# Optimization experiments

Hardware: AMD Instinct MI355X
Metric: run time of the kernel (lower is better)

Reference implementation:

```python
import jax, jax.numpy as jnp
import numpy as np

B, T, D, H = 4, 2048, 1024, 16
HD = D // H  # head_dim = 64


def setup_inputs() -> dict:
    key = jax.random.key(0)
    ks = jax.random.split(key, 7)
    x = jax.random.normal(ks[0], (B, T, D), dtype=jnp.float32)
    engagement = jax.random.uniform(ks[1], (B, T), dtype=jnp.float32)
    mask = jax.random.uniform(ks[2], (B, T)) < 0.1  # True = masked-out key
    s = 1.0 / np.sqrt(D)
    qkv_w = jax.random.normal(ks[3], (3 * D, D), dtype=jnp.float32) * s
    qkv_b = jax.random.normal(ks[4], (3 * D,), dtype=jnp.float32) * 0.02
    out_w = jax.random.normal(ks[5], (D, D), dtype=jnp.float32) * s
    out_b = jax.random.normal(ks[6], (D,), dtype=jnp.float32) * 0.02
    return {"x": x, "engagement": engagement, "mask": mask,
            "qkv_w": qkv_w, "qkv_b": qkv_b, "out_w": out_w, "out_b": out_b}


def reference(x, engagement, mask, qkv_w, qkv_b, out_w, out_b):
    b, t, d = x.shape
    qkv = x @ qkv_w.T + qkv_b                       # [B,T,3D]
    q, k, v = jnp.split(qkv, 3, axis=-1)
    # [B,T,D] -> [B,H,T,HD]
    to_heads = lambda a: a.reshape(b, t, H, HD).transpose(0, 2, 1, 3)
    q, k, v = to_heads(q), to_heads(k), to_heads(v)
    attn = jnp.einsum('bhqd,bhkd->bhqk', q, k) / jnp.sqrt(jnp.float32(HD))
    log_g = jnp.log(jnp.clip(engagement, 1e-6))     # [B,T] per-key bias
    attn = attn + log_g[:, None, None, :]
    attn = jnp.where(mask[:, None, None, :], jnp.float32(-1e9), attn)
    p = jax.nn.softmax(attn, axis=-1)
    o = jnp.einsum('bhqk,bhkd->bhqd', p, v)         # [B,H,T,HD]
    o = o.transpose(0, 2, 1, 3).reshape(b, t, d)    # [B,T,D]
    return o @ out_w.T + out_b
```

## Files before the change

kernel.cpp:

```cpp
#include <hip/hip_runtime.h>
#include <math.h>

#define B_  4
#define T_  2048
#define D_  1024
#define H_  16
#define HD_ 64

typedef unsigned short ushort_t;
typedef unsigned int uint_t;
typedef __attribute__((ext_vector_type(8))) short bf16x8;
typedef __attribute__((ext_vector_type(4))) float f32x4;

#define SC_LOG2 0.1803368801111243f

__device__ inline ushort_t f2bf(float f) {
  uint_t u = __float_as_uint(f);
  u += 0x7fffu + ((u >> 16) & 1u);
  return (ushort_t)(u >> 16);
}
__device__ inline ushort_t f2bf_fast(float f) {
  return (ushort_t)((__float_as_uint(f) + 0x8000u) >> 16);
}

__device__ inline void gload_lds16(const ushort_t* g, ushort_t* l) {
  __builtin_amdgcn_global_load_lds(
      (const __attribute__((address_space(1))) unsigned int*)g,
      (__attribute__((address_space(3))) unsigned int*)l, 16, 0, 0);
}

__global__ __launch_bounds__(256) void cvt_bf16(const float* __restrict__ in,
                                                ushort_t* __restrict__ out, int n) {
  int i = (blockIdx.x * 256 + threadIdx.x) * 4;
  if (i + 3 < n) {
    float4 v = *(const float4*)(in + i);
    uint_t lo = (uint_t)f2bf(v.x) | ((uint_t)f2bf(v.y) << 16);
    uint_t hi = (uint_t)f2bf(v.z) | ((uint_t)f2bf(v.w) << 16);
    *(uint2*)(out + i) = make_uint2(lo, hi);
  }
}

__global__ __launch_bounds__(256) void bias_prep(const float* __restrict__ eng,
                                                 const int* __restrict__ mask,
                                                 float* __restrict__ biasA, int n) {
  int i = blockIdx.x * 256 + threadIdx.x;
  if (i < n) biasA[i] = mask[i] ? -1e30f : __log2f(fmaxf(eng[i], 1e-6f));
}

template <int WRITE_BF16>
__global__ __launch_bounds__(256) void gemm_bf16(
    const ushort_t* __restrict__ A, const ushort_t* __restrict__ Bm,
    const float* __restrict__ bias, void* __restrict__ Cout,
    int M, int N, int K) {
  __shared__ __align__(16) ushort_t Ls[8192];
  ushort_t* As = Ls;
  ushort_t* Bs = Ls + 4096;
  const int tid = threadIdx.x;
  const int w = tid >> 6, lane = tid & 63;
  const int l15 = lane & 15, quad = lane >> 4;
  const int wm = w >> 1, wn = w & 1;
  const int m0 = blockIdx.y * 128, n0 = blockIdx.x * 128;

  f32x4 acc[4][4];
#pragma unroll
  for (int a = 0; a < 4; ++a)
#pragma unroll
    for (int b = 0; b < 4; ++b) acc[a][b] = (f32x4){0.f, 0.f, 0.f, 0.f};

  const int sr = lane >> 2;
  const int gc = (lane & 3) ^ ((sr >> 1) & 3);

  for (int k0 = 0; k0 < K; k0 += 32) {
    __syncthreads();
#pragma unroll
    for (int u = 0; u < 2; ++u) {
      int row = w * 32 + u * 16 + sr;
      gload_lds16(A + (size_t)(m0 + row) * K + k0 + gc * 8,
                  &As[(w * 32 + u * 16) * 32]);
      gload_lds16(Bm + (size_t)(n0 + row) * K + k0 + gc * 8,
                  &Bs[(w * 32 + u * 16) * 32]);
    }
    __syncthreads();
    bf16x8 af[4], bf[4];
#pragma unroll
    for (int mb = 0; mb < 4; ++mb) {
      int row = wm * 64 + mb * 16 + l15;
      int p = quad ^ ((l15 >> 1) & 3);
      af[mb] = *(const bf16x8*)(&As[row * 32 + p * 8]);
    }
#pragma unroll
    for (int nb = 0; nb < 4; ++nb) {
      int row = wn * 64 + nb * 16 + l15;
      int p = quad ^ ((l15 >> 1) & 3);
      bf[nb] = *(const bf16x8*)(&Bs[row * 32 + p * 8]);
    }
#pragma unroll
    for (int mb = 0; mb < 4; ++mb)
#pragma unroll
      for (int nb = 0; nb < 4; ++nb)
        acc[mb][nb] = __builtin_amdgcn_mfma_f32_16x16x32_bf16(
            af[mb], bf[nb], acc[mb][nb], 0, 0, 0);
  }

  float bb[4];
#pragma unroll
  for (int nb = 0; nb < 4; ++nb) bb[nb] = bias[n0 + wn * 64 + nb * 16 + l15];

  if (WRITE_BF16) {
    ushort_t* Cb = (ushort_t*)Cout;
#pragma unroll
    for (int mb = 0; mb < 4; ++mb) {
      __syncthreads();
#pragma unroll
      for (int nb = 0; nb < 4; ++nb)
#pragma unroll
        for (int i = 0; i < 4; ++i) {
          float v = acc[mb][nb][i] + bb[nb];
          Ls[(wm * 16 + quad * 4 + i) * 136 + wn * 64 + nb * 16 + l15] =
              f2bf_fast(v);
        }
      __syncthreads();
      int lr = tid >> 3, c = tid & 7;
      size_t gr = (size_t)(m0 + (lr >> 4) * 64 + mb * 16 + (lr & 15));
      uint4 v0 = *(const uint4*)&Ls[lr * 136 + c * 16];
      uint4 v1 = *(const uint4*)&Ls[lr * 136 + c * 16 + 8];
      *(uint4*)&Cb[gr * N + n0 + c * 16] = v0;
      *(uint4*)&Cb[gr * N + n0 + c * 16 + 8] = v1;
    }
  } else {
    float* Cf = (float*)Cout;
#pragma unroll
    for (int mb = 0; mb < 4; ++mb)
#pragma unroll
      for (int i = 0; i < 4; ++i) {
        size_t row = (size_t)(m0 + wm * 64 + mb * 16 + quad * 4 + i);
#pragma unroll
        for (int nb = 0; nb < 4; ++nb)
          Cf[row * N + n0 + wn * 64 + nb * 16 + l15] = acc[mb][nb][i] + bb[nb];
      }
  }
}

__global__ __launch_bounds__(256) void attn_mfma(
    const ushort_t* __restrict__ qkv, const float* __restrict__ biasA,
    ushort_t* __restrict__ oat) {
  __shared__ __align__(16) ushort_t Kb[64 * 64];
  __shared__ __align__(16) ushort_t Vb[8 * 520];
  __shared__ __align__(16) ushort_t Pl[4][16 * 72];
  __shared__ float bsh[64];

  const int b = blockIdx.z, h = blockIdx.y;
  const int q0 = blockIdx.x * 64;
  const int tid = threadIdx.x;
  const int w = tid >> 6, lane = tid & 63;
  const int l15 = lane & 15, quad = lane >> 4;
  const size_t rs = 3 * D_;

  const ushort_t* qb =
      qkv + (size_t)(b * T_ + q0 + w * 16 + l15) * rs + h * HD_;
  bf16x8 qf0 = *(const bf16x8*)(qb + quad * 8);
  bf16x8 qf1 = *(const bf16x8*)(qb + 32 + quad * 8);

  f32x4 Oa[4];
#pragma unroll
  for (int nb = 0; nb < 4; ++nb) Oa[nb] = (f32x4){0.f, 0.f, 0.f, 0.f};
  float rsum[4] = {0.f, 0.f, 0.f, 0.f};

  const ushort_t* kbase = qkv + (size_t)(b * T_) * rs + D_ + h * HD_;
  const ushort_t* vbase = kbase + D_;
  const float* bptr = biasA + b * T_;
  ushort_t* pw = &Pl[w][0];

  const int kr = lane >> 3, kc = lane & 7;
  const int kgc = kc ^ kr;

  for (int k0 = 0; k0 < T_; k0 += 64) {
    __syncthreads();
#pragma unroll
    for (int u = 0; u < 2; ++u) {
      int key = w * 16 + u * 8 + kr;
      gload_lds16(kbase + (size_t)(k0 + key) * rs + kgc * 8,
                  &Kb[(w * 16 + u * 8) * 64]);
    }
    {
      int kp = tid & 31, c = tid >> 5;
      const ushort_t* v0p = vbase + (size_t)(k0 + 2 * kp) * rs + c * 8;
      uint4 va = *(const uint4*)v0p;
      uint4 vc = *(const uint4*)(v0p + rs);
      uint_t* dst = (uint_t*)&Vb[(kp >> 2) * 520 + c * 64 + 2 * (kp & 3)];
      dst[0]  = (va.x & 0xffffu) | (vc.x << 16);
      dst[4]  = (va.x >> 16)     | (vc.x & 0xffff0000u);
      dst[8]  = (va.y & 0xffffu) | (vc.y << 16);
      dst[12] = (va.y >> 16)     | (vc.y & 0xffff0000u);
      dst[16] = (va.z & 0xffffu) | (vc.z << 16);
      dst[20] = (va.z >> 16)     | (vc.z & 0xffff0000u);
      dst[24] = (va.w & 0xffffu) | (vc.w << 16);
      dst[28] = (va.w >> 16)     | (vc.w & 0xffff0000u);
    }
    if (tid < 64) bsh[tid] = bptr[k0 + tid];
    __syncthreads();

#pragma unroll
    for (int nb = 0; nb < 4; ++nb) {
      int key = nb * 16 + l15;
      int p0 = (quad ^ (key & 7)) * 8;
      bf16x8 kf0 = *(const bf16x8*)(&Kb[key * 64 + p0]);
      bf16x8 kf1 = *(const bf16x8*)(&Kb[key * 64 + (p0 ^ 32)]);
      f32x4 s = (f32x4){0.f, 0.f, 0.f, 0.f};
      s = __builtin_amdgcn_mfma_f32_16x16x32_bf16(qf0, kf0, s, 0, 0, 0);
      s = __builtin_amdgcn_mfma_f32_16x16x32_bf16(qf1, kf1, s, 0, 0, 0);
      float bias2 = bsh[key];
#pragma unroll
      for (int i = 0; i < 4; ++i) {
        float p = __builtin_amdgcn_exp2f(s[i] * SC_LOG2 + bias2);
        rsum[i] += p;
        pw[(quad * 4 + i) * 72 + nb * 16 + l15] = f2bf_fast(p);
      }
    }

    bf16x8 pf0 = *(const bf16x8*)(&pw[l15 * 72 + quad * 8]);
    bf16x8 pf1 = *(const bf16x8*)(&pw[l15 * 72 + 32 + quad * 8]);
#pragma unroll
    for (int nb = 0; nb < 4; ++nb) {
      bf16x8 vf0 = *(const bf16x8*)(&Vb[quad * 520 + (nb * 16 + l15) * 8]);
      bf16x8 vf1 = *(const bf16x8*)(&Vb[(4 + quad) * 520 + (nb * 16 + l15) * 8]);
      Oa[nb] = __builtin_amdgcn_mfma_f32_16x16x32_bf16(pf0, vf0, Oa[nb], 0, 0, 0);
      Oa[nb] = __builtin_amdgcn_mfma_f32_16x16x32_bf16(pf1, vf1, Oa[nb], 0, 0, 0);
    }
  }

  float invl[4];
#pragma unroll
  for (int i = 0; i < 4; ++i) {
    float r = rsum[i];
    r += __shfl_xor(r, 1, 16);
    r += __shfl_xor(r, 2, 16);
    r += __shfl_xor(r, 4, 16);
    r += __shfl_xor(r, 8, 16);
    invl[i] = 1.0f / r;
  }
#pragma unroll
  for (int nb = 0; nb < 4; ++nb)
#pragma unroll
    for (int i = 0; i < 4; ++i)
      pw[(quad * 4 + i) * 72 + nb * 16 + l15] = f2bf_fast(Oa[nb][i] * invl[i]);
  ushort_t* dst = oat + (size_t)(b * T_ + q0 + w * 16) * D_ + h * HD_;
#pragma unroll
  for (int pp = 0; pp < 2; ++pp) {
    int row = pp * 8 + (lane >> 3), c = lane & 7;
    uint4 v = *(const uint4*)&pw[row * 72 + c * 8];
    *(uint4*)&dst[(size_t)row * D_ + c * 8] = v;
  }
}

extern "C" void kernel_launch(void* const* d_in, const int* in_sizes, int n_in,
                              void* d_out, int out_size, void* d_ws, size_t ws_size,
                              hipStream_t stream) {
  const float* x     = (const float*)d_in[0];
  const float* eng   = (const float*)d_in[1];
  const int*   mask  = (const int*)d_in[2];
  const float* qkv_w = (const float*)d_in[3];
  const float* qkv_b = (const float*)d_in[4];
  const float* out_w = (const float*)d_in[5];
  const float* out_b = (const float*)d_in[6];
  float* out = (float*)d_out;

  const int M = B_ * T_;
  const size_t nx = (size_t)M * D_;
  const size_t nwq = (size_t)3 * D_ * D_;
  const size_t nwo = (size_t)D_ * D_;
  const size_t nqkv = (size_t)M * 3 * D_;

  char* p = (char*)d_ws;
  ushort_t* xb    = (ushort_t*)p;            p += nx * 2;
  ushort_t* wqkvb = (ushort_t*)p;            p += nwq * 2;
  ushort_t* woutb = (ushort_t*)p;            p += nwo * 2;
  ushort_t* qkvb  = (ushort_t*)p;            p += nqkv * 2;
  ushort_t* oatb  = (ushort_t*)p;            p += nx * 2;
  float*    biasA = (float*)p;               p += (size_t)M * 4;

  cvt_bf16<<<(int)(nx / 1024), 256, 0, stream>>>(x, xb, (int)nx);
  cvt_bf16<<<(int)(nwq / 1024), 256, 0, stream>>>(qkv_w, wqkvb, (int)nwq);
  cvt_bf16<<<(int)(nwo / 1024), 256, 0, stream>>>(out_w, woutb, (int)nwo);
  bias_prep<<<M / 256, 256, 0, stream>>>(eng, mask, biasA, M);

  gemm_bf16<1><<<dim3(3 * D_ / 128, M / 128), 256, 0, stream>>>(
      xb, wqkvb, qkv_b, qkvb, M, 3 * D_, D_);
  attn_mfma<<<dim3(T_ / 64, H_, B_), 256, 0, stream>>>(qkvb, biasA, oatb);
  gemm_bf16<0><<<dim3(D_ / 128, M / 128), 256, 0, stream>>>(
      oatb, woutb, out_b, out, M, D_, D_);
}
```

Baseline: 352.9 us.

## Keep softmax probabilities in registers via transposed QK^T and double query tile

The attention kernel now processes 128 queries per block (32 per wave, two 16-row sub-tiles), reusing each K/V tile loaded into LDS across twice as many queries. S is computed as K·Q^T so the MFMA output layout matches the A-operand layout for the PV MFMA, which lets probabilities be packed to bf16 in registers instead of round-tripping through LDS. The V LDS layout is permuted to match. K and V fragments are hoisted into registers per tile. Costs: more registers per thread and half as many blocks, which may reduce occupancy.

Measured after the change: 350.1 us. About the same (-0.8%).

```diff
diff --git a/kernel.cpp b/kernel.cpp
--- a/kernel.cpp
+++ b/kernel.cpp
@@ -21,6 +21,11 @@
 }
 __device__ inline ushort_t f2bf_fast(float f) {
   return (ushort_t)((__float_as_uint(f) + 0x8000u) >> 16);
+}
+__device__ inline uint_t pack2bf(float a, float b) {
+  uint_t ua = (__float_as_uint(a) + 0x8000u) >> 16;
+  uint_t ub = (__float_as_uint(b) + 0x8000u) & 0xffff0000u;
+  return ua | ub;
 }
 
 __device__ inline void gload_lds16(const ushort_t* g, ushort_t* l) {
@@ -146,30 +151,36 @@
     ushort_t* __restrict__ oat) {
   __shared__ __align__(16) ushort_t Kb[64 * 64];
   __shared__ __align__(16) ushort_t Vb[8 * 520];
-  __shared__ __align__(16) ushort_t Pl[4][16 * 72];
-  __shared__ float bsh[64];
+  __shared__ __align__(16) float bsh[64];
+  __shared__ __align__(16) float lsum[4][32];
+  __shared__ __align__(16) ushort_t Ost[4][32 * 72];
 
   const int b = blockIdx.z, h = blockIdx.y;
-  const int q0 = blockIdx.x * 64;
+  const int q0 = blockIdx.x * 128;
   const int tid = threadIdx.x;
   const int w = tid >> 6, lane = tid & 63;
   const int l15 = lane & 15, quad = lane >> 4;
   const size_t rs = 3 * D_;
 
-  const ushort_t* qb =
-      qkv + (size_t)(b * T_ + q0 + w * 16 + l15) * rs + h * HD_;
-  bf16x8 qf0 = *(const bf16x8*)(qb + quad * 8);
-  bf16x8 qf1 = *(const bf16x8*)(qb + 32 + quad * 8);
-
-  f32x4 Oa[4];
-#pragma unroll
-  for (int nb = 0; nb < 4; ++nb) Oa[nb] = (f32x4){0.f, 0.f, 0.f, 0.f};
-  float rsum[4] = {0.f, 0.f, 0.f, 0.f};
+  bf16x8 qf[2][2];
+#pragma unroll
+  for (int qb = 0; qb < 2; ++qb) {
+    const ushort_t* qp =
+        qkv + (size_t)(b * T_ + q0 + w * 32 + qb * 16 + l15) * rs + h * HD_;
+    qf[qb][0] = *(const bf16x8*)(qp + quad * 8);
+    qf[qb][1] = *(const bf16x8*)(qp + 32 + quad * 8);
+  }
+
+  f32x4 Oa[2][4];
+#pragma unroll
+  for (int qb = 0; qb < 2; ++qb)
+#pragma unroll
+    for (int nb = 0; nb < 4; ++nb) Oa[qb][nb] = (f32x4){0.f, 0.f, 0.f, 0.f};
+  float rsum[2] = {0.f, 0.f};
 
   const ushort_t* kbase = qkv + (size_t)(b * T_) * rs + D_ + h * HD_;
   const ushort_t* vbase = kbase + D_;
   const float* bptr = biasA + b * T_;
-  ushort_t* pw = &Pl[w][0];
 
   const int kr = lane >> 3, kc = lane & 7;
   const int kgc = kc ^ kr;
@@ -187,7 +198,9 @@
       const ushort_t* v0p = vbase + (size_t)(k0 + 2 * kp) * rs + c * 8;
       uint4 va = *(const uint4*)v0p;
       uint4 vc = *(const uint4*)(v0p + rs);
-      uint_t* dst = (uint_t*)&Vb[(kp >> 2) * 520 + c * 64 + 2 * (kp & 3)];
+      int gp = (kp >> 4) * 4 + ((kp >> 1) & 3);
+      int j0 = ((kp >> 3) & 1) * 4 + 2 * (kp & 1);
+      uint_t* dst = (uint_t*)&Vb[gp * 520 + c * 64 + j0];
       dst[0]  = (va.x & 0xffffu) | (vc.x << 16);
       dst[4]  = (va.x >> 16)     | (vc.x & 0xffff0000u);
       dst[8]  = (va.y & 0xffffu) | (vc.y << 16);
@@ -200,55 +213,88 @@
     if (tid < 64) bsh[tid] = bptr[k0 + tid];
     __syncthreads();
 
+    bf16x8 kf0[4], kf1[4];
 #pragma unroll
     for (int nb = 0; nb < 4; ++nb) {
       int key = nb * 16 + l15;
       int p0 = (quad ^ (key & 7)) * 8;
-      bf16x8 kf0 = *(const bf16x8*)(&Kb[key * 64 + p0]);
-      bf16x8 kf1 = *(const bf16x8*)(&Kb[key * 64 + (p0 ^ 32)]);
-      f32x4 s = (f32x4){0.f, 0.f, 0.f, 0.f};
-      s = __builtin_amdgcn_mfma_f32_16x16x32_bf16(qf0, kf0, s, 0, 0, 0);
-      s = __builtin_amdgcn_mfma_f32_16x16x32_bf16(qf1, kf1, s, 0, 0, 0);
-      float bias2 = bsh[key];
-#pragma unroll
-      for (int i = 0; i < 4; ++i) {
-        float p = __builtin_amdgcn_exp2f(s[i] * SC_LOG2 + bias2);
-        rsum[i] += p;
-        pw[(quad * 4 + i) * 72 + nb * 16 + l15] = f2bf_fast(p);
+      kf0[nb] = *(const bf16x8*)(&Kb[key * 64 + p0]);
+      kf1[nb] = *(const bf16x8*)(&Kb[key * 64 + (p0 ^ 32)]);
+    }
+    bf16x8 vf0[4], vf1[4];
+#pragma unroll
+    for (int nbd = 0; nbd < 4; ++nbd) {
+      vf0[nbd] = *(const bf16x8*)(&Vb[quad * 520 + (nbd * 16 + l15) * 8]);
+      vf1[nbd] = *(const bf16x8*)(&Vb[(4 + quad) * 520 + (nbd * 16 + l15) * 8]);
+    }
+
+#pragma unroll
+    for (int qb = 0; qb < 2; ++qb) {
+      f32x4 st[4];
+#pragma unroll
+      for (int nb = 0; nb < 4; ++nb) {
+        f32x4 s = (f32x4){0.f, 0.f, 0.f, 0.f};
+        s = __builtin_amdgcn_mfma_f32_16x16x32_bf16(kf0[nb], qf[qb][0], s, 0, 0, 0);
+        s = __builtin_amdgcn_mfma_f32_16x16x32_bf16(kf1[nb], qf[qb][1], s, 0, 0, 0);
+        st[nb] = s;
       }
-    }
-
-    bf16x8 pf0 = *(const bf16x8*)(&pw[l15 * 72 + quad * 8]);
-    bf16x8 pf1 = *(const bf16x8*)(&pw[l15 * 72 + 32 + quad * 8]);
-#pragma unroll
-    for (int nb = 0; nb < 4; ++nb) {
-      bf16x8 vf0 = *(const bf16x8*)(&Vb[quad * 520 + (nb * 16 + l15) * 8]);
-      bf16x8 vf1 = *(const bf16x8*)(&Vb[(4 + quad) * 520 + (nb * 16 + l15) * 8]);
-      Oa[nb] = __builtin_amdgcn_mfma_f32_16x16x32_bf16(pf0, vf0, Oa[nb], 0, 0, 0);
-      Oa[nb] = __builtin_amdgcn_mfma_f32_16x16x32_bf16(pf1, vf1, Oa[nb], 0, 0, 0);
-    }
-  }
-
-  float invl[4];
-#pragma unroll
-  for (int i = 0; i < 4; ++i) {
-    float r = rsum[i];
-    r += __shfl_xor(r, 1, 16);
-    r += __shfl_xor(r, 2, 16);
-    r += __shfl_xor(r, 4, 16);
-    r += __shfl_xor(r, 8, 16);
-    invl[i] = 1.0f / r;
-  }
-#pragma unroll
-  for (int nb = 0; nb < 4; ++nb)
-#pragma unroll
-    for (int i = 0; i < 4; ++i)
-      pw[(quad * 4 + i) * 72 + nb * 16 + l15] = f2bf_fast(Oa[nb][i] * invl[i]);
-  ushort_t* dst = oat + (size_t)(b * T_ + q0 + w * 16) * D_ + h * HD_;
-#pragma unroll
-  for (int pp = 0; pp < 2; ++pp) {
+      float pp[4][4];
+      float racc = 0.f;
+#pragma unroll
+      for (int nb = 0; nb < 4; ++nb) {
+        f32x4 bv = *(const f32x4*)&bsh[nb * 16 + quad * 4];
+#pragma unroll
+        for (int i = 0; i < 4; ++i) {
+          float p = __builtin_amdgcn_exp2f(st[nb][i] * SC_LOG2 + bv[i]);
+          pp[nb][i] = p;
+          racc += p;
+        }
+      }
+      rsum[qb] += racc;
+      union { uint4 u; bf16x8 v; } pf0, pf1;
+      pf0.u.x = pack2bf(pp[0][0], pp[0][1]);
+      pf0.u.y = pack2bf(pp[0][2], pp[0][3]);
+      pf0.u.z = pack2bf(pp[1][0], pp[1][1]);
+      pf0.u.w = pack2bf(pp[1][2], pp[1][3]);
+      pf1.u.x = pack2bf(pp[2][0], pp[2][1]);
+      pf1.u.y = pack2bf(pp[2][2], pp[2][3]);
+      pf1.u.z = pack2bf(pp[3][0], pp[3][1]);
+      pf1.u.w = pack2bf(pp[3][2], pp[3][3]);
+#pragma unroll
+      for (int nbd = 0; nbd < 4; ++nbd) {
+        Oa[qb][nbd] = __builtin_amdgcn_mfma_f32_16x16x32_bf16(
+            pf0.v, vf0[nbd], Oa[qb][nbd], 0, 0, 0);
+        Oa[qb][nbd] = __builtin_amdgcn_mfma_f32_16x16x32_bf16(
+            pf1.v, vf1[nbd], Oa[qb][nbd], 0, 0, 0);
+      }
+    }
+  }
+
+#pragma unroll
+  for (int qb = 0; qb < 2; ++qb) {
+    float r = rsum[qb];
+    r += __shfl_xor(r, 16, 64);
+    r += __shfl_xor(r, 32, 64);
+    if (lane < 16) lsum[w][qb * 16 + lane] = r;
+  }
+#pragma unroll
+  for (int qb = 0; qb < 2; ++qb) {
+    f32x4 lr = *(const f32x4*)&lsum[w][qb * 16 + quad * 4];
+    f32x4 invl;
+#pragma unroll
+    for (int i = 0; i < 4; ++i) invl[i] = 1.0f / lr[i];
+#pragma unroll
+    for (int nbd = 0; nbd < 4; ++nbd)
+#pragma unroll
+      for (int i = 0; i < 4; ++i)
+        Ost[w][(qb * 16 + quad * 4 + i) * 72 + nbd * 16 + l15] =
+            f2bf_fast(Oa[qb][nbd][i] * invl[i]);
+  }
+  ushort_t* dst = oat + (size_t)(b * T_ + q0 + w * 32) * D_ + h * HD_;
+#pragma unroll
+  for (int pp = 0; pp < 4; ++pp) {
     int row = pp * 8 + (lane >> 3), c = lane & 7;
-    uint4 v = *(const uint4*)&pw[row * 72 + c * 8];
+    uint4 v = *(const uint4*)&Ost[w][row * 72 + c * 8];
     *(uint4*)&dst[(size_t)row * D_ + c * 8] = v;
   }
 }
@@ -286,7 +332,7 @@
 
   gemm_bf16<1><<<dim3(3 * D_ / 128, M / 128), 256, 0, stream>>>(
       xb, wqkvb, qkv_b, qkvb, M, 3 * D_, D_);
-  attn_mfma<<<dim3(T_ / 64, H_, B_), 256, 0, stream>>>(qkvb, biasA, oatb);
+  attn_mfma<<<dim3(T_ / 128, H_, B_), 256, 0, stream>>>(qkvb, biasA, oatb);
   gemm_bf16<0><<<dim3(D_ / 128, M / 128), 256, 0, stream>>>(
       oatb, woutb, out_b, out, M, D_, D_);
 }
```
